# Kernel tuning notes

Hardware: AMD Instinct MI355X
Metric: run time of the kernel (lower is better)

## Reference

```python
import jax, jax.numpy as jnp
import numpy as np

INTER = 128  # inter_channels


def _proj(x, W, b, s, t):
    # 1x1 conv (channels-first) + eval-mode BN (folded to per-channel affine) + ReLU
    y = jnp.einsum('bchw,oc->bohw', x, W) + b[None, :, None, None]
    return jax.nn.relu(y * s[None, :, None, None] + t[None, :, None, None])


def setup_inputs() -> dict:
    key = jax.random.key(0)
    ks = jax.random.split(key, 16)
    B, C, H, Wd = 4, 256, 64, 64
    OUT = 256
    d = {}
    d['x1'] = jax.random.normal(ks[0], (B, C, H, Wd), jnp.float32)
    d['x2'] = jax.random.normal(ks[1], (B, C, H, Wd), jnp.float32)

    def mk(i, oc, ic):
        W = jax.random.normal(ks[i], (oc, ic), jnp.float32) * (ic ** -0.5)
        b = jnp.zeros((oc,), jnp.float32)
        s = jax.random.uniform(ks[i + 1], (oc,), jnp.float32, 0.5, 1.5)
        t = jax.random.normal(ks[i + 2], (oc,), jnp.float32) * 0.1
        return W, b, s, t

    d['Wq'], d['bq'], d['sq'], d['tq'] = mk(2, INTER, C)
    d['Wk'], d['bk'], d['sk'], d['tk'] = mk(5, INTER, C)
    d['Wv'], d['bv'], d['sv'], d['tv'] = mk(8, INTER, C)
    d['Wp'], d['bp'], d['sp'], d['tp'] = mk(11, OUT, 2 * INTER)
    return d


def reference(x1, x2, Wq, bq, sq, tq, Wk, bk, sk, tk, Wv, bv, sv, tv, Wp, bp, sp, tp):
    B, _, H, Wd = x1.shape
    N = H * Wd
    # projections; shared to_value applied to both x1 and x2 (as in original)
    q1 = _proj(x1, Wq, bq, sq, tq).reshape(B, INTER, N).transpose(0, 2, 1)  # b n c
    k2 = _proj(x2, Wk, bk, sk, tk).reshape(B, INTER, N)                      # b c m
    v1 = _proj(x1, Wv, bv, sv, tv).reshape(B, INTER, N).transpose(0, 2, 1)  # b m c
    v2 = _proj(x2, Wv, bv, sv, tv).reshape(B, INTER, N).transpose(0, 2, 1)  # b m c
    dots = jnp.einsum('bnc,bcm->bnm', q1, k2) * (INTER ** -0.5)
    A = 1.0 - jax.nn.softmax(dots, axis=-1)  # post-softmax complement attention
    out1 = jnp.einsum('bnm,bmc->bnc', A, v2)
    out2 = jnp.einsum('bnm,bmc->bnc', A, v1)
    out = jnp.concatenate([out1, out2], axis=-1)            # b n 2c
    out = out.transpose(0, 2, 1).reshape(B, 2 * INTER, H, Wd)
    return _proj(out, Wp, bp, sp, tp)
```

## Files before the change

kernel.cpp:

```cpp
#include <hip/hip_runtime.h>

#define B_ 4
#define C_ 256
#define CI_ 128
#define N_ 4096
#define OC_ 256

typedef __bf16 bf16x8 __attribute__((ext_vector_type(8)));
typedef float f32x4 __attribute__((ext_vector_type(4)));

#define MFMA16(a, b, c) __builtin_amdgcn_mfma_f32_16x16x32_bf16((a), (b), (c), 0, 0, 0)

__device__ __forceinline__ unsigned f2bf(float f) {
  unsigned u = __float_as_uint(f);
  return (u + 0x7fffu + ((u >> 16) & 1u)) >> 16;
}
__device__ __forceinline__ float b2f(unsigned h) { return __uint_as_float(h << 16); }
__device__ __forceinline__ bf16x8 ld8(const unsigned short* p) {
  return *reinterpret_cast<const bf16x8*>(p);
}
__device__ __forceinline__ void gll16(const void* g, void* l) {
  __builtin_amdgcn_global_load_lds((const __attribute__((address_space(1))) void*)g,
                                   (__attribute__((address_space(3))) void*)l, 16, 0, 0);
}

__global__ __launch_bounds__(256) void dpf_tkern(const float* __restrict__ x1,
                                                 const float* __restrict__ x2,
                                                 unsigned short* __restrict__ xt) {
  __shared__ float lt[64][65];
  int bid = blockIdx.x;
  int src = bid >> 10, rem = bid & 1023;
  int b = rem >> 8, ct = (rem >> 6) & 3, nt = rem & 63;
  const float* x = src ? x2 : x1;
  unsigned short* dst = xt + (size_t)src * ((size_t)B_ * N_ * C_);
  int t = threadIdx.x;
  int cl = t >> 2, nlo = (t & 3) << 4;
  const float* rp = x + ((size_t)(b * C_ + ct * 64 + cl)) * N_ + nt * 64 + nlo;
#pragma unroll
  for (int q = 0; q < 4; ++q) {
    float4 v = *reinterpret_cast<const float4*>(rp + q * 4);
    lt[cl][nlo + q * 4 + 0] = v.x;
    lt[cl][nlo + q * 4 + 1] = v.y;
    lt[cl][nlo + q * 4 + 2] = v.z;
    lt[cl][nlo + q * 4 + 3] = v.w;
  }
  __syncthreads();
  int nl = t & 63, cb = (t >> 6) << 4;
  unsigned h[16];
#pragma unroll
  for (int q = 0; q < 16; ++q) h[q] = f2bf(lt[cb + q][nl]);
  uint4 u0, u1;
  u0.x = h[0] | (h[1] << 16); u0.y = h[2] | (h[3] << 16);
  u0.z = h[4] | (h[5] << 16); u0.w = h[6] | (h[7] << 16);
  u1.x = h[8] | (h[9] << 16); u1.y = h[10] | (h[11] << 16);
  u1.z = h[12] | (h[13] << 16); u1.w = h[14] | (h[15] << 16);
  unsigned short* op = dst + ((size_t)(b * N_ + nt * 64 + nl)) * C_ + ct * 64 + cb;
  *reinterpret_cast<uint4*>(op) = u0;
  *reinterpret_cast<uint4*>(op + 8) = u1;
}

__global__ __launch_bounds__(256) void dpf_wckern(
    const float* __restrict__ Wq, const float* __restrict__ Wk, const float* __restrict__ Wv,
    const float* __restrict__ Wp, unsigned short* __restrict__ Wqb, unsigned short* __restrict__ Wkb,
    unsigned short* __restrict__ Wvb, unsigned short* __restrict__ Wpb) {
  int bid = blockIdx.x;
  const float* src;
  unsigned short* dst;
  int lb;
  if (bid < 16) { src = Wq; dst = Wqb; lb = bid; }
  else if (bid < 32) { src = Wk; dst = Wkb; lb = bid - 16; }
  else if (bid < 48) { src = Wv; dst = Wvb; lb = bid - 32; }
  else { src = Wp; dst = Wpb; lb = bid - 48; }
  int o = lb * 2048 + threadIdx.x * 8;
  float4 a = *reinterpret_cast<const float4*>(src + o);
  float4 c = *reinterpret_cast<const float4*>(src + o + 4);
  uint4 u;
  u.x = f2bf(a.x) | (f2bf(a.y) << 16);
  u.y = f2bf(a.z) | (f2bf(a.w) << 16);
  u.z = f2bf(c.x) | (f2bf(c.y) << 16);
  u.w = f2bf(c.z) | (f2bf(c.w) << 16);
  *reinterpret_cast<uint4*>(dst + o) = u;
}

__global__ __launch_bounds__(256, 2) void dpf_pkern(
    const unsigned short* __restrict__ Xt, const unsigned short* __restrict__ Wqb,
    const unsigned short* __restrict__ Wkb, const unsigned short* __restrict__ Wvb,
    const float* __restrict__ bq, const float* __restrict__ sq, const float* __restrict__ tq,
    const float* __restrict__ bk, const float* __restrict__ sk, const float* __restrict__ tk,
    const float* __restrict__ bv, const float* __restrict__ sv, const float* __restrict__ tv,
    unsigned short* __restrict__ Qg, unsigned short* __restrict__ Kt,
    unsigned short* __restrict__ Vt) {
  int bid = blockIdx.x;
  int g = bid >> 7, b = (bid >> 5) & 3, nt = bid & 31;
  int n0 = nt * 128;
  int t = threadIdx.x, lane = t & 63, wid = t >> 6;
  int wo = wid >> 1, wn = wid & 1;
  int lrow = lane & 15, lhi = lane >> 4;

  const unsigned short* W = (g == 0) ? Wqb : (g == 1) ? Wkb : Wvb;
  const unsigned short* X = Xt + ((g == 0 || g == 2) ? (size_t)0 : (size_t)B_ * N_ * C_);
  const float* bb = (g == 0) ? bq : (g == 1) ? bk : bv;
  const float* ss = (g == 0) ? sq : (g == 1) ? sk : sv;
  const float* tt = (g == 0) ? tq : (g == 1) ? tk : tv;
  const float extra = (g < 2) ? 0.29730177875068026f : 1.0f;

  f32x4 acc[4][4];
#pragma unroll
  for (int i = 0; i < 4; ++i)
#pragma unroll
    for (int jj = 0; jj < 4; ++jj) acc[i][jj] = (f32x4){0.f, 0.f, 0.f, 0.f};

  const unsigned short* wbase = W + (size_t)(64 * wo + lrow) * C_ + 8 * lhi;
  const unsigned short* xbase = X + ((size_t)(b * N_ + n0 + 64 * wn + lrow)) * C_ + 8 * lhi;

  for (int ks = 0; ks < 8; ++ks) {
    bf16x8 wf[4], xf[4];
#pragma unroll
    for (int of = 0; of < 4; ++of) wf[of] = ld8(wbase + (size_t)(16 * of) * C_ + 32 * ks);
#pragma unroll
    for (int nf = 0; nf < 4; ++nf) xf[nf] = ld8(xbase + (size_t)(16 * nf) * C_ + 32 * ks);
    if (g < 2) {
#pragma unroll
      for (int of = 0; of < 4; ++of)
#pragma unroll
        for (int nf = 0; nf < 4; ++nf) acc[of][nf] = MFMA16(wf[of], xf[nf], acc[of][nf]);
    } else {
#pragma unroll
      for (int of = 0; of < 4; ++of)
#pragma unroll
        for (int nf = 0; nf < 4; ++nf) acc[of][nf] = MFMA16(xf[nf], wf[of], acc[of][nf]);
    }
  }

  if (g < 2) {
#pragma unroll
    for (int of = 0; of < 4; ++of) {
      int ob = 64 * wo + 16 * of + 4 * lhi;
      float4 s4 = *reinterpret_cast<const float4*>(ss + ob);
      float4 b4 = *reinterpret_cast<const float4*>(bb + ob);
      float4 t4 = *reinterpret_cast<const float4*>(tt + ob);
      float sc0 = s4.x * extra, sc1 = s4.y * extra, sc2 = s4.z * extra, sc3 = s4.w * extra;
      float sh0 = (b4.x * s4.x + t4.x) * extra, sh1 = (b4.y * s4.y + t4.y) * extra;
      float sh2 = (b4.z * s4.z + t4.z) * extra, sh3 = (b4.w * s4.w + t4.w) * extra;
#pragma unroll
      for (int nf = 0; nf < 4; ++nf) {
        int n = n0 + 64 * wn + 16 * nf + lrow;
        float y0 = fmaxf(acc[of][nf][0] * sc0 + sh0, 0.f);
        float y1 = fmaxf(acc[of][nf][1] * sc1 + sh1, 0.f);
        float y2 = fmaxf(acc[of][nf][2] * sc2 + sh2, 0.f);
        float y3 = fmaxf(acc[of][nf][3] * sc3 + sh3, 0.f);
        uint2 pk;
        pk.x = f2bf(y0) | (f2bf(y1) << 16);
        pk.y = f2bf(y2) | (f2bf(y3) << 16);
        if (g == 0) {
          *reinterpret_cast<uint2*>(Qg + ((size_t)(b * N_ + n)) * CI_ + ob) = pk;
        } else {
          size_t idx = (size_t)b * 524288 + (size_t)n * 128 + (ob ^ ((n & 15) << 3));
          *reinterpret_cast<uint2*>(Kt + idx) = pk;
        }
      }
    }
  } else {
    int vs = (g == 2) ? 1 : 0;
#pragma unroll
    for (int of = 0; of < 4; ++of) {
      int o = 64 * wo + 16 * of + lrow;
      float sc = ss[o];
      float sh = bb[o] * sc + tt[o];
#pragma unroll
      for (int nf = 0; nf < 4; ++nf) {
        int nb = n0 + 64 * wn + 16 * nf + 4 * lhi;
        float y0 = fmaxf(acc[of][nf][0] * sc + sh, 0.f);
        float y1 = fmaxf(acc[of][nf][1] * sc + sh, 0.f);
        float y2 = fmaxf(acc[of][nf][2] * sc + sh, 0.f);
        float y3 = fmaxf(acc[of][nf][3] * sc + sh, 0.f);
        uint2 pk;
        pk.x = f2bf(y0) | (f2bf(y1) << 16);
        pk.y = f2bf(y2) | (f2bf(y3) << 16);
        size_t idx = (size_t)b * 1048576 + (size_t)(nb >> 7) * 32768 + (size_t)vs * 16384 +
                     (size_t)o * 128 + ((nb & 127) ^ ((o & 15) << 3));
        *reinterpret_cast<uint2*>(Vt + idx) = pk;
      }
    }
  }
}

__global__ __launch_bounds__(256) void dpf_cskern(const unsigned short* __restrict__ Vt,
                                                  float* __restrict__ colsum) {
  __shared__ float ps[4];
  int bid = blockIdx.x;
  int vs = bid >> 9, b = (bid >> 7) & 3, c = bid & 127;
  int t = threadIdx.x;
  const unsigned short* src = Vt + (size_t)b * 1048576 + (size_t)(t >> 3) * 32768 +
                              (size_t)vs * 16384 + (size_t)c * 128 + (t & 7) * 16;
  float s = 0.f;
#pragma unroll
  for (int i = 0; i < 2; ++i) {
    uint4 u = *reinterpret_cast<const uint4*>(src + i * 8);
    s += b2f(u.x & 0xffffu) + b2f(u.x >> 16) + b2f(u.y & 0xffffu) + b2f(u.y >> 16);
    s += b2f(u.z & 0xffffu) + b2f(u.z >> 16) + b2f(u.w & 0xffffu) + b2f(u.w >> 16);
  }
#pragma unroll
  for (int off = 1; off < 64; off <<= 1) s += __shfl_xor(s, off, 64);
  if ((t & 63) == 0) ps[t >> 6] = s;
  __syncthreads();
  if (t == 0) colsum[vs * 512 + b * 128 + c] = ps[0] + ps[1] + ps[2] + ps[3];
}

__global__ __launch_bounds__(512)
__attribute__((amdgpu_waves_per_eu(2, 2))) void dpf_akern(
    const unsigned short* __restrict__ Qg, const unsigned short* __restrict__ Kt,
    const unsigned short* __restrict__ Vt, const float* __restrict__ colsum,
    unsigned short* __restrict__ Cat) {
  extern __shared__ char smem[];
  unsigned short(*lP)[32][40] = reinterpret_cast<unsigned short(*)[32][40]>(smem + 131072);
  float* mb = reinterpret_cast<float*>(smem);

  const float L2E = 1.44269504088896f;
  int t = threadIdx.x, lane = t & 63, wid = t >> 6;
  int g = wid >> 1, j = wid & 1;
  int lrow = lane & 15, lhi = lane >> 4;
  int swz = lrow << 3;

  int bid = blockIdx.x;
  int xcd = bid & 7;
  int b = xcd >> 1;
  int qt = ((bid >> 3) << 1) | (xcd & 1);
  int n0 = qt * 64;

  bf16x8 qf[2][4];
#pragma unroll
  for (int nf = 0; nf < 2; ++nf) {
    const unsigned short* qp = Qg + ((size_t)(b * N_ + n0 + 32 * j + 16 * nf + lrow)) * CI_ + 8 * lhi;
#pragma unroll
    for (int ks = 0; ks < 4; ++ks) qf[nf][ks] = ld8(qp + 32 * ks);
  }

  f32x4 acc[2][2][8];
#pragma unroll
  for (int nf = 0; nf < 2; ++nf)
#pragma unroll
    for (int vs = 0; vs < 2; ++vs)
#pragma unroll
      for (int cf = 0; cf < 8; ++cf) acc[nf][vs][cf] = (f32x4){0.f, 0.f, 0.f, 0.f};
  float mrun[2] = {-1e30f, -1e30f}, lrun[2] = {0.f, 0.f};

  const char* kb = (const char*)Kt + (size_t)b * 1048576 + wid * 4096 + lane * 16;
  const char* vb = (const char*)Vt + (size_t)b * 2097152 + wid * 8192 + lane * 16;

#pragma unroll
  for (int e = 0; e < 4; ++e) gll16(kb + e * 1024, smem + (wid * 4 + e) * 1024);
  __syncthreads();

  int cur = 0;
#pragma unroll 1
  for (int step = 0; step < 32; ++step) {
    const char* vsrc = vb + (size_t)step * 65536;
#pragma unroll
    for (int e = 0; e < 8; ++e) gll16(vsrc + e * 1024, smem + 65536 + (wid * 8 + e) * 1024);
    const char* ksrc = kb + (size_t)((step + 1) & 31) * 32768;
#pragma unroll
    for (int e = 0; e < 4; ++e)
      gll16(ksrc + e * 1024, smem + (cur ^ 1) * 32768 + (wid * 4 + e) * 1024);

    const unsigned short* lk = (const unsigned short*)(smem + cur * 32768);
    f32x4 sacc[2][2];
#pragma unroll
    for (int nf = 0; nf < 2; ++nf)
#pragma unroll
      for (int mf = 0; mf < 2; ++mf) sacc[nf][mf] = (f32x4){0.f, 0.f, 0.f, 0.f};
    __builtin_amdgcn_s_setprio(1);
#pragma unroll
    for (int ks = 0; ks < 4; ++ks) {
      int ci = (32 * ks + 8 * lhi) ^ swz;
      bf16x8 kf0 = ld8(lk + (32 * g + lrow) * 128 + ci);
      bf16x8 kf1 = ld8(lk + (32 * g + 16 + lrow) * 128 + ci);
#pragma unroll
      for (int nf = 0; nf < 2; ++nf) {
        sacc[nf][0] = MFMA16(kf0, qf[nf][ks], sacc[nf][0]);
        sacc[nf][1] = MFMA16(kf1, qf[nf][ks], sacc[nf][1]);
      }
    }
    __builtin_amdgcn_s_setprio(0);

#pragma unroll
    for (int nf = 0; nf < 2; ++nf) {
      float smax = fmaxf(fmaxf(fmaxf(sacc[nf][0][0], sacc[nf][0][1]), fmaxf(sacc[nf][0][2], sacc[nf][0][3])),
                         fmaxf(fmaxf(sacc[nf][1][0], sacc[nf][1][1]), fmaxf(sacc[nf][1][2], sacc[nf][1][3])));
      smax = fmaxf(smax, __shfl_xor(smax, 16, 64));
      smax = fmaxf(smax, __shfl_xor(smax, 32, 64));
      if (!__all(smax - mrun[nf] <= 8.0f)) {
        float mnew = fmaxf(mrun[nf], smax);
        float fsc = __builtin_amdgcn_exp2f((mrun[nf] - mnew) * L2E);
        mrun[nf] = mnew;
        lrun[nf] *= fsc;
#pragma unroll
        for (int vs = 0; vs < 2; ++vs)
#pragma unroll
          for (int cf = 0; cf < 8; ++cf) acc[nf][vs][cf] *= fsc;
      }
      float p[2][4];
      float ls = 0.f;
#pragma unroll
      for (int mf = 0; mf < 2; ++mf)
#pragma unroll
        for (int r = 0; r < 4; ++r) {
          p[mf][r] = __builtin_amdgcn_exp2f((sacc[nf][mf][r] - mrun[nf]) * L2E);
          ls += p[mf][r];
        }
      ls += __shfl_xor(ls, 16, 64);
      ls += __shfl_xor(ls, 32, 64);
      lrun[nf] += ls;
#pragma unroll
      for (int mf = 0; mf < 2; ++mf) {
        uint2 pk;
        pk.x = f2bf(p[mf][0]) | (f2bf(p[mf][1]) << 16);
        pk.y = f2bf(p[mf][2]) | (f2bf(p[mf][3]) << 16);
        *reinterpret_cast<uint2*>(&lP[wid][16 * nf + lrow][16 * mf + 4 * lhi]) = pk;
      }
    }

    asm volatile("s_waitcnt vmcnt(4)\ns_barrier" ::: "memory");

    const unsigned short* lv = (const unsigned short*)(smem + 65536);
    bf16x8 pf0 = ld8(&lP[wid][lrow][8 * lhi]);
    bf16x8 pf1 = ld8(&lP[wid][16 + lrow][8 * lhi]);
    int mi = (32 * g + 8 * lhi) ^ swz;
    __builtin_amdgcn_s_setprio(1);
#pragma unroll
    for (int vs = 0; vs < 2; ++vs)
#pragma unroll
      for (int cf = 0; cf < 8; ++cf) {
        bf16x8 vf = ld8(lv + (vs * 128 + 16 * cf + lrow) * 128 + mi);
        acc[0][vs][cf] = MFMA16(vf, pf0, acc[0][vs][cf]);
        acc[1][vs][cf] = MFMA16(vf, pf1, acc[1][vs][cf]);
      }
    __builtin_amdgcn_s_setprio(0);
    __syncthreads();
    cur ^= 1;
  }
  __syncthreads();

  auto wstate = [&](int s) {
    float* base = mb + (size_t)s * (132 * 64) + lane;
    base[0] = mrun[0]; base[64] = lrun[0]; base[128] = mrun[1]; base[192] = lrun[1];
#pragma unroll
    for (int nf = 0; nf < 2; ++nf)
#pragma unroll
      for (int vs = 0; vs < 2; ++vs)
#pragma unroll
        for (int cf = 0; cf < 8; ++cf)
#pragma unroll
          for (int r = 0; r < 4; ++r)
            base[(4 + ((nf * 2 + vs) * 8 + cf) * 4 + r) * 64] = acc[nf][vs][cf][r];
  };
  auto mstate = [&](int s) {
    float* base = mb + (size_t)s * (132 * 64) + lane;
    float a0[2], a1[2];
#pragma unroll
    for (int nf = 0; nf < 2; ++nf) {
      float m2 = base[(2 * nf) * 64], l2 = base[(2 * nf + 1) * 64];
      float M = fmaxf(mrun[nf], m2);
      a0[nf] = __builtin_amdgcn_exp2f((mrun[nf] - M) * L2E);
      a1[nf] = __builtin_amdgcn_exp2f((m2 - M) * L2E);
      lrun[nf] = lrun[nf] * a0[nf] + l2 * a1[nf];
      mrun[nf] = M;
    }
#pragma unroll
    for (int nf = 0; nf < 2; ++nf)
#pragma unroll
      for (int vs = 0; vs < 2; ++vs)
#pragma unroll
        for (int cf = 0; cf < 8; ++cf)
#pragma unroll
          for (int r = 0; r < 4; ++r)
            acc[nf][vs][cf][r] = acc[nf][vs][cf][r] * a0[nf] +
                                 base[(4 + ((nf * 2 + vs) * 8 + cf) * 4 + r) * 64] * a1[nf];
  };

  if (g == 1) wstate(j);
  if (g == 3) wstate(2 + j);
  __syncthreads();
  if (g == 0) mstate(j);
  if (g == 2) mstate(2 + j);
  __syncthreads();
  if (g == 2) wstate(j);
  __syncthreads();
  if (g == 0) {
    mstate(j);
    float inv[2] = {1.0f / lrun[0], 1.0f / lrun[1]};
#pragma unroll
    for (int nf = 0; nf < 2; ++nf) {
#pragma unroll
      for (int vs = 0; vs < 2; ++vs) {
#pragma unroll
        for (int cf = 0; cf < 8; ++cf) {
          int cb = 16 * cf + 4 * lhi;
          float4 cs = *reinterpret_cast<const float4*>(colsum + vs * 512 + b * 128 + cb);
          float y0 = cs.x - acc[nf][vs][cf][0] * inv[nf];
          float y1 = cs.y - acc[nf][vs][cf][1] * inv[nf];
          float y2 = cs.z - acc[nf][vs][cf][2] * inv[nf];
          float y3 = cs.w - acc[nf][vs][cf][3] * inv[nf];
          uint2 pk;
          pk.x = f2bf(y0) | (f2bf(y1) << 16);
          pk.y = f2bf(y2) | (f2bf(y3) << 16);
          *reinterpret_cast<uint2*>(Cat + ((size_t)(b * N_ + n0 + 32 * j + 16 * nf + lrow)) * OC_ +
                                    vs * 128 + cb) = pk;
        }
      }
    }
  }
}

__global__ __launch_bounds__(256, 2) void dpf_fkern(const unsigned short* __restrict__ Cat,
                                                    const unsigned short* __restrict__ Wpb,
                                                    const float* __restrict__ bp,
                                                    const float* __restrict__ sp,
                                                    const float* __restrict__ tp,
                                                    float* __restrict__ out) {
  int bid = blockIdx.x;
  int b = bid >> 6, nt = bid & 63;
  int n0 = nt * 64;
  int t = threadIdx.x, lane = t & 63, wid = t >> 6;
  int lrow = lane & 15, lhi = lane >> 4;
  f32x4 acc[4][4];
#pragma unroll
  for (int i = 0; i < 4; ++i)
#pragma unroll
    for (int jj = 0; jj < 4; ++jj) acc[i][jj] = (f32x4){0.f, 0.f, 0.f, 0.f};
  const unsigned short* cbase = Cat + ((size_t)(b * N_ + n0 + lrow)) * OC_ + 8 * lhi;
  const unsigned short* wbase = Wpb + (size_t)(64 * wid + lrow) * OC_ + 8 * lhi;
  for (int ks = 0; ks < 8; ++ks) {
    bf16x8 af[4], bfv[4];
#pragma unroll
    for (int nf = 0; nf < 4; ++nf) af[nf] = ld8(cbase + (size_t)(16 * nf) * OC_ + 32 * ks);
#pragma unroll
    for (int of = 0; of < 4; ++of) bfv[of] = ld8(wbase + (size_t)(16 * of) * OC_ + 32 * ks);
#pragma unroll
    for (int nf = 0; nf < 4; ++nf)
#pragma unroll
      for (int of = 0; of < 4; ++of) acc[nf][of] = MFMA16(af[nf], bfv[of], acc[nf][of]);
  }
#pragma unroll
  for (int of = 0; of < 4; ++of) {
    int o = 64 * wid + 16 * of + lrow;
    float sc = sp[o];
    float sh = bp[o] * sc + tp[o];
#pragma unroll
    for (int nf = 0; nf < 4; ++nf) {
      float4 y;
      y.x = fmaxf(acc[nf][of][0] * sc + sh, 0.f);
      y.y = fmaxf(acc[nf][of][1] * sc + sh, 0.f);
      y.z = fmaxf(acc[nf][of][2] * sc + sh, 0.f);
      y.w = fmaxf(acc[nf][of][3] * sc + sh, 0.f);
      *reinterpret_cast<float4*>(out + ((size_t)(b * OC_ + o)) * N_ + n0 + 16 * nf + 4 * lhi) = y;
    }
  }
}

extern "C" void kernel_launch(void* const* d_in, const int* in_sizes, int n_in, void* d_out,
                              int out_size, void* d_ws, size_t ws_size, hipStream_t stream) {
  (void)in_sizes; (void)n_in; (void)out_size; (void)ws_size;
  const float* x1 = (const float*)d_in[0];
  const float* x2 = (const float*)d_in[1];
  const float* Wq = (const float*)d_in[2];
  const float* bq = (const float*)d_in[3];
  const float* sq = (const float*)d_in[4];
  const float* tq = (const float*)d_in[5];
  const float* Wk = (const float*)d_in[6];
  const float* bk = (const float*)d_in[7];
  const float* sk = (const float*)d_in[8];
  const float* tk = (const float*)d_in[9];
  const float* Wv = (const float*)d_in[10];
  const float* bv = (const float*)d_in[11];
  const float* sv = (const float*)d_in[12];
  const float* tv = (const float*)d_in[13];
  const float* Wp = (const float*)d_in[14];
  const float* bp = (const float*)d_in[15];
  const float* sp = (const float*)d_in[16];
  const float* tp = (const float*)d_in[17];

  char* w = (char*)d_ws;
  size_t o = 0;
  unsigned short* Xt = (unsigned short*)(w + o);  o += (size_t)2 * B_ * N_ * C_ * 2;
  unsigned short* Wqb = (unsigned short*)(w + o); o += (size_t)128 * 256 * 2;
  unsigned short* Wkb = (unsigned short*)(w + o); o += (size_t)128 * 256 * 2;
  unsigned short* Wvb = (unsigned short*)(w + o); o += (size_t)128 * 256 * 2;
  unsigned short* Wpb = (unsigned short*)(w + o); o += (size_t)256 * 256 * 2;
  unsigned short* Qg = (unsigned short*)(w + o);  o += (size_t)B_ * N_ * CI_ * 2;
  unsigned short* Kt = (unsigned short*)(w + o);  o += (size_t)B_ * N_ * CI_ * 2;
  unsigned short* Vt = (unsigned short*)(w + o);  o += (size_t)2 * B_ * N_ * CI_ * 2;
  unsigned short* Cat = (unsigned short*)(w + o); o += (size_t)B_ * N_ * OC_ * 2;
  float* csum = (float*)(w + o);                  o += (size_t)2 * B_ * CI_ * 4;

  dpf_tkern<<<2048, 256, 0, stream>>>(x1, x2, Xt);
  dpf_wckern<<<80, 256, 0, stream>>>(Wq, Wk, Wv, Wp, Wqb, Wkb, Wvb, Wpb);
  dpf_pkern<<<512, 256, 0, stream>>>(Xt, Wqb, Wkb, Wvb, bq, sq, tq, bk, sk, tk, bv, sv, tv,
                                     Qg, Kt, Vt);
  dpf_cskern<<<1024, 256, 0, stream>>>(Vt, csum);
  dpf_akern<<<256, 512, 151552, stream>>>(Qg, Kt, Vt, csum, Cat);
  dpf_fkern<<<256, 256, 0, stream>>>(Cat, Wpb, bp, sp, tp, (float*)d_out);
}
```

Before: 239.0 us.

## Load V directly into registers, split attention work across waves by key range

V is now stored in plain channel-major layout and each wave loads its V fragments straight from global memory into registers, no longer staging them through LDS. The work split also changes: each wave group now handles a key sub-range for both value streams, and P tiles plus per-row rescale factors are shared through double-buffered LDS. Per-wave softmax max/sum states are merged once at the end with a simple add reduction. Separately, the final projection kernel stages its output tile in LDS so the global stores are coalesced. The intent is to cut LDS traffic and barriers in the main loop, at the cost of more direct global loads and extra LDS handoff of P and scale factors.

```diff
diff --git a/kernel.cpp b/kernel.cpp
--- a/kernel.cpp
+++ b/kernel.cpp
@@ -177,8 +177,7 @@
         uint2 pk;
         pk.x = f2bf(y0) | (f2bf(y1) << 16);
         pk.y = f2bf(y2) | (f2bf(y3) << 16);
-        size_t idx = (size_t)b * 1048576 + (size_t)(nb >> 7) * 32768 + (size_t)vs * 16384 +
-                     (size_t)o * 128 + ((nb & 127) ^ ((o & 15) << 3));
+        size_t idx = ((size_t)((b * 2 + vs) * CI_ + o)) * (size_t)N_ + nb;
         *reinterpret_cast<uint2*>(Vt + idx) = pk;
       }
     }
@@ -191,12 +190,11 @@
   int bid = blockIdx.x;
   int vs = bid >> 9, b = (bid >> 7) & 3, c = bid & 127;
   int t = threadIdx.x;
-  const unsigned short* src = Vt + (size_t)b * 1048576 + (size_t)(t >> 3) * 32768 +
-                              (size_t)vs * 16384 + (size_t)c * 128 + (t & 7) * 16;
+  const unsigned short* src = Vt + ((size_t)((b * 2 + vs) * CI_ + c)) * (size_t)N_;
   float s = 0.f;
 #pragma unroll
   for (int i = 0; i < 2; ++i) {
-    uint4 u = *reinterpret_cast<const uint4*>(src + i * 8);
+    uint4 u = *reinterpret_cast<const uint4*>(src + t * 8 + i * 2048);
     s += b2f(u.x & 0xffffu) + b2f(u.x >> 16) + b2f(u.y & 0xffffu) + b2f(u.y >> 16);
     s += b2f(u.z & 0xffffu) + b2f(u.z >> 16) + b2f(u.w & 0xffffu) + b2f(u.w >> 16);
   }
@@ -213,7 +211,11 @@
     const unsigned short* __restrict__ Vt, const float* __restrict__ colsum,
     unsigned short* __restrict__ Cat) {
   extern __shared__ char smem[];
-  unsigned short(*lP)[32][40] = reinterpret_cast<unsigned short(*)[32][40]>(smem + 131072);
+  unsigned short(*lPd)[8][32][40] = reinterpret_cast<unsigned short(*)[8][32][40]>(smem + 65536);
+  float* fscL = reinterpret_cast<float*>(smem + 106496);
+  int* flagL = reinterpret_cast<int*>(smem + 108544);
+  float* SLm = reinterpret_cast<float*>(smem + 131072);
+  float* SLl = reinterpret_cast<float*>(smem + 132096);
   float* mb = reinterpret_cast<float*>(smem);
 
   const float L2E = 1.44269504088896f;
@@ -238,32 +240,37 @@
 
   f32x4 acc[2][2][8];
 #pragma unroll
-  for (int nf = 0; nf < 2; ++nf)
-#pragma unroll
-    for (int vs = 0; vs < 2; ++vs)
-#pragma unroll
-      for (int cf = 0; cf < 8; ++cf) acc[nf][vs][cf] = (f32x4){0.f, 0.f, 0.f, 0.f};
+  for (int jj = 0; jj < 2; ++jj)
+#pragma unroll
+    for (int nf = 0; nf < 2; ++nf)
+#pragma unroll
+      for (int cf = 0; cf < 8; ++cf) acc[jj][nf][cf] = (f32x4){0.f, 0.f, 0.f, 0.f};
   float mrun[2] = {-1e30f, -1e30f}, lrun[2] = {0.f, 0.f};
 
   const char* kb = (const char*)Kt + (size_t)b * 1048576 + wid * 4096 + lane * 16;
-  const char* vb = (const char*)Vt + (size_t)b * 2097152 + wid * 8192 + lane * 16;
-
-#pragma unroll
-  for (int e = 0; e < 4; ++e) gll16(kb + e * 1024, smem + (wid * 4 + e) * 1024);
-  __syncthreads();
-
-  int cur = 0;
+  const unsigned short* vbase = Vt + (size_t)(b * 2 + j) * 524288 + (size_t)lrow * (size_t)N_ +
+                                32 * g + 8 * lhi;
+
+#pragma unroll
+  for (int e = 0; e < 4; ++e) gll16(kb + e * 1024, smem + wid * 4096 + e * 1024);
+  asm volatile("s_waitcnt vmcnt(0)" ::: "memory");
+  __builtin_amdgcn_s_barrier();
+
 #pragma unroll 1
   for (int step = 0; step < 32; ++step) {
-    const char* vsrc = vb + (size_t)step * 65536;
-#pragma unroll
-    for (int e = 0; e < 8; ++e) gll16(vsrc + e * 1024, smem + 65536 + (wid * 8 + e) * 1024);
+    int p = step & 1;
     const char* ksrc = kb + (size_t)((step + 1) & 31) * 32768;
 #pragma unroll
     for (int e = 0; e < 4; ++e)
-      gll16(ksrc + e * 1024, smem + (cur ^ 1) * 32768 + (wid * 4 + e) * 1024);
-
-    const unsigned short* lk = (const unsigned short*)(smem + cur * 32768);
+      gll16(ksrc + e * 1024, smem + (p ^ 1) * 32768 + wid * 4096 + e * 1024);
+    asm volatile("s_waitcnt vmcnt(4)" ::: "memory");
+
+    const unsigned short* vstep = vbase + step * 128;
+    bf16x8 vreg[8];
+#pragma unroll
+    for (int cf = 0; cf < 8; ++cf) vreg[cf] = ld8(vstep + (size_t)cf * 65536);
+
+    const unsigned short* lk = (const unsigned short*)(smem + p * 32768);
     f32x4 sacc[2][2];
 #pragma unroll
     for (int nf = 0; nf < 2; ++nf)
@@ -289,24 +296,22 @@
                          fmaxf(fmaxf(sacc[nf][1][0], sacc[nf][1][1]), fmaxf(sacc[nf][1][2], sacc[nf][1][3])));
       smax = fmaxf(smax, __shfl_xor(smax, 16, 64));
       smax = fmaxf(smax, __shfl_xor(smax, 32, 64));
-      if (!__all(smax - mrun[nf] <= 8.0f)) {
+      int doresc = !__all(smax - mrun[nf] <= 8.0f);
+      float fsc = 1.0f;
+      if (doresc) {
         float mnew = fmaxf(mrun[nf], smax);
-        float fsc = __builtin_amdgcn_exp2f((mrun[nf] - mnew) * L2E);
+        fsc = __builtin_amdgcn_exp2f((mrun[nf] - mnew) * L2E);
         mrun[nf] = mnew;
         lrun[nf] *= fsc;
-#pragma unroll
-        for (int vs = 0; vs < 2; ++vs)
-#pragma unroll
-          for (int cf = 0; cf < 8; ++cf) acc[nf][vs][cf] *= fsc;
-      }
-      float p[2][4];
+      }
       float ls = 0.f;
 #pragma unroll
       for (int mf = 0; mf < 2; ++mf)
 #pragma unroll
         for (int r = 0; r < 4; ++r) {
-          p[mf][r] = __builtin_amdgcn_exp2f((sacc[nf][mf][r] - mrun[nf]) * L2E);
-          ls += p[mf][r];
+          float pv = __builtin_amdgcn_exp2f((sacc[nf][mf][r] - mrun[nf]) * L2E);
+          sacc[nf][mf][r] = pv;
+          ls += pv;
         }
       ls += __shfl_xor(ls, 16, 64);
       ls += __shfl_xor(ls, 32, 64);
@@ -314,101 +319,127 @@
 #pragma unroll
       for (int mf = 0; mf < 2; ++mf) {
         uint2 pk;
-        pk.x = f2bf(p[mf][0]) | (f2bf(p[mf][1]) << 16);
-        pk.y = f2bf(p[mf][2]) | (f2bf(p[mf][3]) << 16);
-        *reinterpret_cast<uint2*>(&lP[wid][16 * nf + lrow][16 * mf + 4 * lhi]) = pk;
-      }
-    }
-
-    asm volatile("s_waitcnt vmcnt(4)\ns_barrier" ::: "memory");
-
-    const unsigned short* lv = (const unsigned short*)(smem + 65536);
-    bf16x8 pf0 = ld8(&lP[wid][lrow][8 * lhi]);
-    bf16x8 pf1 = ld8(&lP[wid][16 + lrow][8 * lhi]);
-    int mi = (32 * g + 8 * lhi) ^ swz;
+        pk.x = f2bf(sacc[nf][mf][0]) | (f2bf(sacc[nf][mf][1]) << 16);
+        pk.y = f2bf(sacc[nf][mf][2]) | (f2bf(sacc[nf][mf][3]) << 16);
+        *reinterpret_cast<uint2*>(&lPd[p][wid][16 * nf + lrow][16 * mf + 4 * lhi]) = pk;
+      }
+      if (lane < 16) fscL[p * 256 + ((g * 2 + j) * 2 + nf) * 16 + lrow] = fsc;
+      if (lane == 0) flagL[p * 16 + (g * 2 + j) * 2 + nf] = doresc;
+    }
+    asm volatile("s_waitcnt lgkmcnt(0)\ns_barrier" ::: "memory");
+
+#pragma unroll
+    for (int jj = 0; jj < 2; ++jj)
+#pragma unroll
+      for (int nf = 0; nf < 2; ++nf) {
+        if (flagL[p * 16 + (g * 2 + jj) * 2 + nf]) {
+          float fs = fscL[p * 256 + ((g * 2 + jj) * 2 + nf) * 16 + lrow];
+#pragma unroll
+          for (int cf = 0; cf < 8; ++cf) acc[jj][nf][cf] *= fs;
+        }
+      }
+    bf16x8 pfr[2][2];
+#pragma unroll
+    for (int jj = 0; jj < 2; ++jj)
+#pragma unroll
+      for (int nf = 0; nf < 2; ++nf)
+        pfr[jj][nf] = ld8(&lPd[p][g * 2 + jj][16 * nf + lrow][8 * lhi]);
     __builtin_amdgcn_s_setprio(1);
 #pragma unroll
-    for (int vs = 0; vs < 2; ++vs)
-#pragma unroll
-      for (int cf = 0; cf < 8; ++cf) {
-        bf16x8 vf = ld8(lv + (vs * 128 + 16 * cf + lrow) * 128 + mi);
-        acc[0][vs][cf] = MFMA16(vf, pf0, acc[0][vs][cf]);
-        acc[1][vs][cf] = MFMA16(vf, pf1, acc[1][vs][cf]);
+    for (int cf = 0; cf < 8; ++cf)
+#pragma unroll
+      for (int jj = 0; jj < 2; ++jj) {
+        acc[jj][0][cf] = MFMA16(vreg[cf], pfr[jj][0], acc[jj][0][cf]);
+        acc[jj][1][cf] = MFMA16(vreg[cf], pfr[jj][1], acc[jj][1][cf]);
       }
     __builtin_amdgcn_s_setprio(0);
-    __syncthreads();
-    cur ^= 1;
-  }
-  __syncthreads();
-
-  auto wstate = [&](int s) {
-    float* base = mb + (size_t)s * (132 * 64) + lane;
-    base[0] = mrun[0]; base[64] = lrun[0]; base[128] = mrun[1]; base[192] = lrun[1];
-#pragma unroll
-    for (int nf = 0; nf < 2; ++nf)
-#pragma unroll
-      for (int vs = 0; vs < 2; ++vs)
+  }
+
+  __syncthreads();
+
+  if (lane < 16) {
+#pragma unroll
+    for (int nf = 0; nf < 2; ++nf) {
+      SLm[((g * 2 + j) * 2 + nf) * 16 + lrow] = mrun[nf];
+      SLl[((g * 2 + j) * 2 + nf) * 16 + lrow] = lrun[nf];
+    }
+  }
+  __syncthreads();
+
+  float invL[2][2];
+#pragma unroll
+  for (int jj = 0; jj < 2; ++jj)
+#pragma unroll
+    for (int nf = 0; nf < 2; ++nf) {
+      float m0_ = SLm[((0 + jj) * 2 + nf) * 16 + lrow];
+      float m1_ = SLm[((2 + jj) * 2 + nf) * 16 + lrow];
+      float m2_ = SLm[((4 + jj) * 2 + nf) * 16 + lrow];
+      float m3_ = SLm[((6 + jj) * 2 + nf) * 16 + lrow];
+      float M = fmaxf(fmaxf(m0_, m1_), fmaxf(m2_, m3_));
+      float a0 = __builtin_amdgcn_exp2f((m0_ - M) * L2E);
+      float a1 = __builtin_amdgcn_exp2f((m1_ - M) * L2E);
+      float a2 = __builtin_amdgcn_exp2f((m2_ - M) * L2E);
+      float a3 = __builtin_amdgcn_exp2f((m3_ - M) * L2E);
+      float L = a0 * SLl[((0 + jj) * 2 + nf) * 16 + lrow] +
+                a1 * SLl[((2 + jj) * 2 + nf) * 16 + lrow] +
+                a2 * SLl[((4 + jj) * 2 + nf) * 16 + lrow] +
+                a3 * SLl[((6 + jj) * 2 + nf) * 16 + lrow];
+      float aown = (g == 0) ? a0 : (g == 1) ? a1 : (g == 2) ? a2 : a3;
+#pragma unroll
+      for (int cf = 0; cf < 8; ++cf) acc[jj][nf][cf] *= aown;
+      invL[jj][nf] = 1.0f / L;
+    }
+
+  auto writeacc = [&](int s) {
+    float* base = mb + s * 8192 + lane * 4;
+#pragma unroll
+    for (int jj = 0; jj < 2; ++jj)
+#pragma unroll
+      for (int nf = 0; nf < 2; ++nf)
 #pragma unroll
         for (int cf = 0; cf < 8; ++cf)
-#pragma unroll
-          for (int r = 0; r < 4; ++r)
-            base[(4 + ((nf * 2 + vs) * 8 + cf) * 4 + r) * 64] = acc[nf][vs][cf][r];
+          *reinterpret_cast<f32x4*>(base + ((jj * 2 + nf) * 8 + cf) * 256) = acc[jj][nf][cf];
   };
-  auto mstate = [&](int s) {
-    float* base = mb + (size_t)s * (132 * 64) + lane;
-    float a0[2], a1[2];
-#pragma unroll
-    for (int nf = 0; nf < 2; ++nf) {
-      float m2 = base[(2 * nf) * 64], l2 = base[(2 * nf + 1) * 64];
-      float M = fmaxf(mrun[nf], m2);
-      a0[nf] = __builtin_amdgcn_exp2f((mrun[nf] - M) * L2E);
-      a1[nf] = __builtin_amdgcn_exp2f((m2 - M) * L2E);
-      lrun[nf] = lrun[nf] * a0[nf] + l2 * a1[nf];
-      mrun[nf] = M;
-    }
-#pragma unroll
-    for (int nf = 0; nf < 2; ++nf)
-#pragma unroll
-      for (int vs = 0; vs < 2; ++vs)
+  auto addacc = [&](int s) {
+    float* base = mb + s * 8192 + lane * 4;
+#pragma unroll
+    for (int jj = 0; jj < 2; ++jj)
+#pragma unroll
+      for (int nf = 0; nf < 2; ++nf)
 #pragma unroll
         for (int cf = 0; cf < 8; ++cf)
-#pragma unroll
-          for (int r = 0; r < 4; ++r)
-            acc[nf][vs][cf][r] = acc[nf][vs][cf][r] * a0[nf] +
-                                 base[(4 + ((nf * 2 + vs) * 8 + cf) * 4 + r) * 64] * a1[nf];
+          acc[jj][nf][cf] += *reinterpret_cast<const f32x4*>(base + ((jj * 2 + nf) * 8 + cf) * 256);
   };
-
-  if (g == 1) wstate(j);
-  if (g == 3) wstate(2 + j);
-  __syncthreads();
-  if (g == 0) mstate(j);
-  if (g == 2) mstate(2 + j);
-  __syncthreads();
-  if (g == 2) wstate(j);
+  if (g == 1) writeacc(j);
+  if (g == 3) writeacc(2 + j);
+  __syncthreads();
+  if (g == 0) addacc(j);
+  if (g == 2) addacc(2 + j);
+  __syncthreads();
+  if (g == 2) writeacc(j);
   __syncthreads();
   if (g == 0) {
-    mstate(j);
-    float inv[2] = {1.0f / lrun[0], 1.0f / lrun[1]};
-#pragma unroll
-    for (int nf = 0; nf < 2; ++nf) {
-#pragma unroll
-      for (int vs = 0; vs < 2; ++vs) {
+    addacc(j);
+#pragma unroll
+    for (int jj = 0; jj < 2; ++jj)
+#pragma unroll
+      for (int nf = 0; nf < 2; ++nf) {
+        float il = invL[jj][nf];
 #pragma unroll
         for (int cf = 0; cf < 8; ++cf) {
           int cb = 16 * cf + 4 * lhi;
-          float4 cs = *reinterpret_cast<const float4*>(colsum + vs * 512 + b * 128 + cb);
-          float y0 = cs.x - acc[nf][vs][cf][0] * inv[nf];
-          float y1 = cs.y - acc[nf][vs][cf][1] * inv[nf];
-          float y2 = cs.z - acc[nf][vs][cf][2] * inv[nf];
-          float y3 = cs.w - acc[nf][vs][cf][3] * inv[nf];
+          float4 cs = *reinterpret_cast<const float4*>(colsum + j * 512 + b * 128 + cb);
+          float y0 = cs.x - acc[jj][nf][cf][0] * il;
+          float y1 = cs.y - acc[jj][nf][cf][1] * il;
+          float y2 = cs.z - acc[jj][nf][cf][2] * il;
+          float y3 = cs.w - acc[jj][nf][cf][3] * il;
           uint2 pk;
           pk.x = f2bf(y0) | (f2bf(y1) << 16);
           pk.y = f2bf(y2) | (f2bf(y3) << 16);
-          *reinterpret_cast<uint2*>(Cat + ((size_t)(b * N_ + n0 + 32 * j + 16 * nf + lrow)) * OC_ +
-                                    vs * 128 + cb) = pk;
+          *reinterpret_cast<uint2*>(Cat + ((size_t)(b * N_ + n0 + 32 * jj + 16 * nf + lrow)) * OC_ +
+                                    j * 128 + cb) = pk;
         }
       }
-    }
   }
 }
 
@@ -418,6 +449,7 @@
                                                     const float* __restrict__ sp,
                                                     const float* __restrict__ tp,
                                                     float* __restrict__ out) {
+  __shared__ float ldsO[256][68];
   int bid = blockIdx.x;
   int b = bid >> 6, nt = bid & 63;
   int n0 = nt * 64;
@@ -453,8 +485,15 @@
       y.y = fmaxf(acc[nf][of][1] * sc + sh, 0.f);
       y.z = fmaxf(acc[nf][of][2] * sc + sh, 0.f);
       y.w = fmaxf(acc[nf][of][3] * sc + sh, 0.f);
-      *reinterpret_cast<float4*>(out + ((size_t)(b * OC_ + o)) * N_ + n0 + 16 * nf + 4 * lhi) = y;
-    }
+      *reinterpret_cast<float4*>(&ldsO[o][16 * nf + 4 * lhi]) = y;
+    }
+  }
+  __syncthreads();
+#pragma unroll
+  for (int pass = 0; pass < 16; ++pass) {
+    int o = pass * 16 + (t >> 4);
+    float4 v = *reinterpret_cast<const float4*>(&ldsO[o][(t & 15) * 4]);
+    *reinterpret_cast<float4*>(out + ((size_t)(b * OC_ + o)) * N_ + n0 + (t & 15) * 4) = v;
   }
 }
 
@@ -498,6 +537,6 @@
   dpf_pkern<<<512, 256, 0, stream>>>(Xt, Wqb, Wkb, Wvb, bq, sq, tq, bk, sk, tk, bv, sv, tv,
                                      Qg, Kt, Vt);
   dpf_cskern<<<1024, 256, 0, stream>>>(Vt, csum);
-  dpf_akern<<<256, 512, 151552, stream>>>(Qg, Kt, Vt, csum, Cat);
+  dpf_akern<<<256, 512, 133120, stream>>>(Qg, Kt, Vt, csum, Cat);
   dpf_fkern<<<256, 256, 0, stream>>>(Cat, Wpb, bp, sp, tp, (float*)d_out);
 }
```

New measurement: 273.5 us. 1.14x slower.
